# Kernel tuning notes

Hardware: AMD Instinct MI355X
Metric: run time of the kernel (lower is better)

The kernel has to match this reference:

```python
import jax, jax.numpy as jnp
import numpy as np

N = 100000   # nodes
E = 1600000  # edges
H = 2        # heads
F = 64       # out_feats per head
D = 256      # node feature dim
DE = 8       # edge feature dim
NEG_SLOPE = 0.2


def setup_inputs() -> dict:
    key = jax.random.key(0)
    ks = jax.random.split(key, 12)
    s = 0.05
    return {
        "feat_src": jax.random.normal(ks[0], (N, D), jnp.float32),
        "feat_edge": jax.random.normal(ks[1], (E, DE), jnp.float32),
        "edge_src": jax.random.randint(ks[2], (E,), 0, N, jnp.int32),
        "edge_dst": jax.random.randint(ks[3], (E,), 0, N, jnp.int32),
        "W_src": jax.random.normal(ks[4], (H * F, D), jnp.float32) * s,
        "W_dst": jax.random.normal(ks[5], (H * F, D), jnp.float32) * s,
        "b_dst": jax.random.normal(ks[6], (H * F,), jnp.float32) * s,
        "W_attn_src": jax.random.normal(ks[7], (H, D), jnp.float32) * s,
        "W_attn_dst": jax.random.normal(ks[8], (H, D), jnp.float32) * s,
        "W_attn_edge": jax.random.normal(ks[9], (H, DE), jnp.float32) * s,
        "W_ngnn": jax.random.normal(ks[10], (H * F, H * F), jnp.float32) * s,
        "b_ngnn": jax.random.normal(ks[11], (H * F,), jnp.float32) * s,
    }


def reference(feat_src, feat_edge, edge_src, edge_dst,
              W_src, W_dst, b_dst, W_attn_src, W_attn_dst, W_attn_edge,
              W_ngnn, b_ngnn):
    # node projections (graph is not a block -> feat_dst = feat_src)
    h_src = (feat_src @ W_src.T).reshape(N, H, F)          # [N,H,F]
    h_dst = (feat_src @ W_dst.T + b_dst).reshape(N, H, F)  # residual branch

    # per-node attention logits [N,H]
    a_src = feat_src @ W_attn_src.T
    a_dst = feat_src @ W_attn_dst.T
    a_edge = feat_edge @ W_attn_edge.T                     # [E,H]

    # per-edge score: u_add_v + edge term, LeakyReLU
    e = a_src[edge_src] + a_dst[edge_dst] + a_edge         # [E,H]
    e = jnp.where(e >= 0, e, NEG_SLOPE * e)

    # edge softmax over incoming edges of each destination node
    m = jax.ops.segment_max(e, edge_dst, num_segments=N)   # [N,H]
    ex = jnp.exp(e - m[edge_dst])
    z = jax.ops.segment_sum(ex, edge_dst, num_segments=N)  # [N,H]
    a = ex / z[edge_dst]                                   # [E,H]

    # weighted gather-scatter aggregation: u_mul_e -> sum per dst
    msg = h_src[edge_src] * a[:, :, None]                  # [E,H,F]
    rst = jax.ops.segment_sum(msg, edge_dst, num_segments=N)  # [N,H,F]

    # ngnn layer + ReLU
    rst = rst.reshape(N, H * F)
    rst = jax.nn.relu(rst @ W_ngnn.T + b_ngnn)
    rst = rst.reshape(N, H, F)

    # residual connection via dst_fc
    rst = rst + h_dst
    return rst
```

## Files before the change

kernel.cpp:

```cpp
#include <hip/hip_runtime.h>
#include <hip/hip_bf16.h>
#include <math.h>

#define NN 100000
#define EE 1600000
#define DD 256
#define DEE 8
#define HF 128
#define NEG_SLOPE 0.2f
#define NBUCK 196
#define P1_EPB 2048
#define P1_TPB 512
#define P1_ITER (P1_EPB / P1_TPB)

typedef __bf16 bf16x8 __attribute__((ext_vector_type(8)));
typedef float  f32x4  __attribute__((ext_vector_type(4)));

__device__ inline ushort f2bf(float f) {
    uint32_t x = __builtin_bit_cast(uint32_t, f);
    x += 0x7fffu + ((x >> 16) & 1u);
    return (ushort)(x >> 16);
}
__device__ inline float bf2f(ushort u) {
    uint32_t x = ((uint32_t)u) << 16;
    return __builtin_bit_cast(float, x);
}
__device__ inline float u2f(uint u) { return __builtin_bit_cast(float, u); }
__device__ inline uint f2u(float f) { return __builtin_bit_cast(uint, f); }
__device__ inline float lo_bf(uint p) { return __builtin_bit_cast(float, p << 16); }
__device__ inline float hi_bf(uint p) { return __builtin_bit_cast(float, p & 0xffff0000u); }

__device__ inline void load_lds16(const void* g, void* l) {
    __builtin_amdgcn_global_load_lds(
        (const __attribute__((address_space(1))) void*)g,
        (__attribute__((address_space(3))) void*)l, 16, 0, 0);
}

__global__ __launch_bounds__(256) void f2bf3_kernel(
    const float* __restrict__ wa, const float* __restrict__ wb,
    const float* __restrict__ wc,
    ushort* __restrict__ oa, ushort* __restrict__ ob, ushort* __restrict__ oc)
{
    int i = (blockIdx.x * 256 + threadIdx.x) * 4;
    const int na = HF * DD, nb2 = 2 * HF * DD, nc3 = 2 * HF * DD + HF * HF;
    const float* src; ushort* dst; int o;
    if (i < na)       { src = wa; dst = oa; o = i; }
    else if (i < nb2) { src = wb; dst = ob; o = i - na; }
    else if (i < nc3) { src = wc; dst = oc; o = i - nb2; }
    else return;
    float4 v = *(const float4*)(src + o);
    ushort4 u;
    u.x = f2bf(v.x); u.y = f2bf(v.y); u.z = f2bf(v.z); u.w = f2bf(v.w);
    *(ushort4*)(dst + o) = u;
}

template<int K>
__global__ __launch_bounds__(256) void mfma_gemm_dual(
    const ushort* __restrict__ W0,
    const ushort* __restrict__ W1,
    const ushort* __restrict__ Xb,
    const float*  __restrict__ bias1,
    ushort* __restrict__ out0, ushort* __restrict__ out1)
{
    __shared__ ushort As[2][128 * 32];
    __shared__ ushort Bs[64 * 32];

    const int tid  = threadIdx.x;
    const int lane = tid & 63, wv = tid >> 6;
    const int wm = wv >> 1, wn = wv & 1;
    const int r = lane & 15, quad = lane >> 4;
    const int m0 = blockIdx.x * 64;

    f32x4 acc[2][4][2] = {};

    for (int k0 = 0; k0 < K; k0 += 32) {
#pragma unroll
        for (int t = 0; t < 2; ++t) {
            int is  = wv + t * 4;
            int row = is * 16 + (lane >> 2);
            int ko  = k0 + (lane & 3) * 8;
            load_lds16(W0 + (size_t)row * K + ko, &As[0][is * 512]);
            load_lds16(W1 + (size_t)row * K + ko, &As[1][is * 512]);
        }
        {
            int is  = wv;
            int row = is * 16 + (lane >> 2);
            int ko  = k0 + (lane & 3) * 8;
            int gm = m0 + row; gm = gm < NN ? gm : NN - 1;
            load_lds16(Xb + (size_t)gm * K + ko, &Bs[is * 512]);
        }
        __syncthreads();
        bf16x8 a[2][4], b[2];
#pragma unroll
        for (int i = 0; i < 4; ++i) {
            a[0][i] = __builtin_bit_cast(bf16x8,
                      *(const f32x4*)&As[0][(wm * 64 + i * 16 + r) * 32 + quad * 8]);
            a[1][i] = __builtin_bit_cast(bf16x8,
                      *(const f32x4*)&As[1][(wm * 64 + i * 16 + r) * 32 + quad * 8]);
        }
#pragma unroll
        for (int j = 0; j < 2; ++j)
            b[j] = __builtin_bit_cast(bf16x8,
                   *(const f32x4*)&Bs[(wn * 32 + j * 16 + r) * 32 + quad * 8]);
#pragma unroll
        for (int s = 0; s < 2; ++s)
#pragma unroll
            for (int i = 0; i < 4; ++i)
#pragma unroll
                for (int j = 0; j < 2; ++j)
                    acc[s][i][j] = __builtin_amdgcn_mfma_f32_16x16x32_bf16(
                        a[s][i], b[j], acc[s][i][j], 0, 0, 0);
        __syncthreads();
    }

#pragma unroll
    for (int s = 0; s < 2; ++s) {
        ushort* outp = s ? out1 : out0;
#pragma unroll
        for (int i = 0; i < 4; ++i) {
            int fbase = wm * 64 + i * 16 + quad * 4;
            float4 bv = make_float4(0.f, 0.f, 0.f, 0.f);
            if (s == 1) bv = *(const float4*)(bias1 + fbase);
#pragma unroll
            for (int j = 0; j < 2; ++j) {
                int node = m0 + wn * 32 + j * 16 + r;
                if (node >= NN) continue;
                f32x4 v = acc[s][i][j];
                v[0] += bv.x; v[1] += bv.y; v[2] += bv.z; v[3] += bv.w;
                ushort4 o;
                o.x = f2bf(v[0]); o.y = f2bf(v[1]); o.z = f2bf(v[2]); o.w = f2bf(v[3]);
                *(ushort4*)(outp + (size_t)node * HF + fbase) = o;
            }
        }
    }
}

template<int K>
__global__ __launch_bounds__(256) void mfma_gemm_ngnn(
    const ushort* __restrict__ Wb,
    const ushort* __restrict__ Xb,
    const float*  __restrict__ bias,
    const ushort* __restrict__ resid,
    float* __restrict__ outp)
{
    __shared__ ushort As[128 * 32];
    __shared__ ushort Bs[128 * 32];

    const int tid  = threadIdx.x;
    const int lane = tid & 63, wv = tid >> 6;
    const int wm = wv >> 1, wn = wv & 1;
    const int r = lane & 15, quad = lane >> 4;
    const int m0 = blockIdx.x * 128;

    f32x4 acc[4][4] = {};

    for (int k0 = 0; k0 < K; k0 += 32) {
#pragma unroll
        for (int t = 0; t < 2; ++t) {
            int is  = wv + t * 4;
            int row = is * 16 + (lane >> 2);
            int ko  = k0 + (lane & 3) * 8;
            load_lds16(Wb + (size_t)row * K + ko, &As[is * 512]);
            int gm = m0 + row; gm = gm < NN ? gm : NN - 1;
            load_lds16(Xb + (size_t)gm * K + ko, &Bs[is * 512]);
        }
        __syncthreads();
        bf16x8 a[4], b[4];
#pragma unroll
        for (int i = 0; i < 4; ++i) {
            a[i] = __builtin_bit_cast(bf16x8,
                   *(const f32x4*)&As[(wm * 64 + i * 16 + r) * 32 + quad * 8]);
            b[i] = __builtin_bit_cast(bf16x8,
                   *(const f32x4*)&Bs[(wn * 64 + i * 16 + r) * 32 + quad * 8]);
        }
#pragma unroll
        for (int i = 0; i < 4; ++i)
#pragma unroll
            for (int j = 0; j < 4; ++j)
                acc[i][j] = __builtin_amdgcn_mfma_f32_16x16x32_bf16(
                    a[i], b[j], acc[i][j], 0, 0, 0);
        __syncthreads();
    }

#pragma unroll
    for (int i = 0; i < 4; ++i) {
        int fbase = wm * 64 + i * 16 + quad * 4;
        float4 bv = *(const float4*)(bias + fbase);
#pragma unroll
        for (int j = 0; j < 4; ++j) {
            int node = m0 + wn * 64 + j * 16 + r;
            if (node >= NN) continue;
            f32x4 v = acc[i][j];
            ushort4 rs = *(const ushort4*)(resid + (size_t)node * HF + fbase);
            float4 o;
            o.x = fmaxf(v[0] + bv.x, 0.f) + bf2f(rs.x);
            o.y = fmaxf(v[1] + bv.y, 0.f) + bf2f(rs.y);
            o.z = fmaxf(v[2] + bv.z, 0.f) + bf2f(rs.z);
            o.w = fmaxf(v[3] + bv.w, 0.f) + bf2f(rs.w);
            *(float4*)(outp + (size_t)node * HF + fbase) = o;
        }
    }
}

__global__ __launch_bounds__(256) void attn_logits_kernel(
    const float* __restrict__ feat,
    const float* __restrict__ Was, const float* __restrict__ Wad,
    float* __restrict__ a_src, float* __restrict__ a_dst,
    ushort* __restrict__ feat_bf)
{
    int wave = threadIdx.x >> 6, lane = threadIdx.x & 63;
    int node = blockIdx.x * 4 + wave;
    if (node >= NN) return;
    float4 f = *(const float4*)(feat + (size_t)node * DD + lane * 4);
    ushort4 fb;
    fb.x = f2bf(f.x); fb.y = f2bf(f.y); fb.z = f2bf(f.z); fb.w = f2bf(f.w);
    *(ushort4*)(feat_bf + (size_t)node * DD + lane * 4) = fb;

    float4 w0 = *(const float4*)(Was + 0 * DD + lane * 4);
    float4 w1 = *(const float4*)(Was + 1 * DD + lane * 4);
    float4 w2 = *(const float4*)(Wad + 0 * DD + lane * 4);
    float4 w3 = *(const float4*)(Wad + 1 * DD + lane * 4);
    float p0 = f.x * w0.x + f.y * w0.y + f.z * w0.z + f.w * w0.w;
    float p1 = f.x * w1.x + f.y * w1.y + f.z * w1.z + f.w * w1.w;
    float p2 = f.x * w2.x + f.y * w2.y + f.z * w2.z + f.w * w2.w;
    float p3 = f.x * w3.x + f.y * w3.y + f.z * w3.z + f.w * w3.w;
#pragma unroll
    for (int o = 32; o > 0; o >>= 1) {
        p0 += __shfl_xor(p0, o);
        p1 += __shfl_xor(p1, o);
        p2 += __shfl_xor(p2, o);
        p3 += __shfl_xor(p3, o);
    }
    if (lane == 0) {
        a_src[node * 2 + 0] = p0; a_src[node * 2 + 1] = p1;
        a_dst[node * 2 + 0] = p2; a_dst[node * 2 + 1] = p3;
    }
}

__global__ __launch_bounds__(256) void hist_kernel(
    const int* __restrict__ edge_dst, int* __restrict__ deg)
{
    int i = blockIdx.x * 256 + threadIdx.x;
    if (i < EE) atomicAdd(&deg[edge_dst[i]], 1);
}

#define SCAN_ELEMS 1024
__global__ __launch_bounds__(256) void scan1_kernel(
    const int* __restrict__ deg, int* __restrict__ offsets, int* __restrict__ blockSums)
{
    __shared__ int sd[256];
    int tid = threadIdx.x;
    int base = blockIdx.x * SCAN_ELEMS + tid * 4;
    int v[4];
#pragma unroll
    for (int c = 0; c < 4; ++c) v[c] = (base + c < NN) ? deg[base + c] : 0;
    int tsum = v[0] + v[1] + v[2] + v[3];
    sd[tid] = tsum;
    __syncthreads();
    for (int o = 1; o < 256; o <<= 1) {
        int x = (tid >= o) ? sd[tid - o] : 0;
        __syncthreads();
        sd[tid] += x;
        __syncthreads();
    }
    int excl = sd[tid] - tsum;
    int run = excl;
#pragma unroll
    for (int c = 0; c < 4; ++c) {
        if (base + c < NN) offsets[base + c] = run;
        run += v[c];
    }
    if (tid == 255) blockSums[blockIdx.x] = sd[255];
}

__global__ __launch_bounds__(128) void scan2_kernel(int* __restrict__ blockSums, int nb)
{
    __shared__ int sd[128];
    int tid = threadIdx.x;
    int tv = (tid < nb) ? blockSums[tid] : 0;
    sd[tid] = tv;
    __syncthreads();
    for (int o = 1; o < 128; o <<= 1) {
        int x = (tid >= o) ? sd[tid - o] : 0;
        __syncthreads();
        sd[tid] += x;
        __syncthreads();
    }
    if (tid < nb) blockSums[tid] = sd[tid] - tv;
}

__global__ __launch_bounds__(256) void scan3_kernel(
    int* __restrict__ offsets, const int* __restrict__ blockSums,
    int* __restrict__ bcur)
{
    int tid = threadIdx.x;
    int base = blockIdx.x * SCAN_ELEMS + tid * 4;
    int add = blockSums[blockIdx.x];
#pragma unroll
    for (int c = 0; c < 4; ++c) {
        int idx = base + c;
        if (idx < NN) {
            int v = offsets[idx] + add;
            offsets[idx] = v;
            if ((idx & 511) == 0) bcur[idx >> 9] = v;
        }
    }
    if (blockIdx.x == 0 && tid == 0) offsets[NN] = EE;
}

__global__ __launch_bounds__(P1_TPB) void bucket_scatter_kernel(
    const int* __restrict__ edge_src, const int* __restrict__ edge_dst,
    const float* __restrict__ feat_edge,
    const float* __restrict__ a_src, const float* __restrict__ a_dst,
    const float* __restrict__ Wae,
    int* __restrict__ bcur, uint4* __restrict__ staging)
{
    __shared__ uint4 rec[P1_EPB];
    __shared__ int cnt[256];
    __shared__ int scanv[256];
    __shared__ int cur[256];
    __shared__ int basearr[256];
    __shared__ int wsum[4];

    const int tid = threadIdx.x;
    const int lane = tid & 63;
    const int b0 = blockIdx.x * P1_EPB;

    if (tid < 256) cnt[tid] = 0;
    __syncthreads();

    int sA[P1_ITER], dA[P1_ITER];
#pragma unroll
    for (int j = 0; j < P1_ITER; ++j) {
        int i = b0 + j * P1_TPB + tid;
        int s = 0, d = 0;
        if (i < EE) {
            s = edge_src[i];
            d = edge_dst[i];
            atomicAdd(&cnt[d >> 9], 1);
        }
        sA[j] = s; dA[j] = d;
    }
    __syncthreads();

    int c = (tid < 256) ? cnt[tid] : 0;
    int x = c;
#pragma unroll
    for (int o = 1; o < 64; o <<= 1) {
        int y = __shfl_up(x, o);
        if (lane >= o) x += y;
    }
    if (tid < 256 && lane == 63) wsum[tid >> 6] = x;
    __syncthreads();
    if (tid < 256) {
        int w4 = tid >> 6;
        int add = 0;
        if (w4 > 0) add += wsum[0];
        if (w4 > 1) add += wsum[1];
        if (w4 > 2) add += wsum[2];
        int excl = x - c + add;
        cur[tid]   = excl;
        scanv[tid] = excl;
        if (tid < NBUCK) basearr[tid] = c ? atomicAdd(&bcur[tid], c) : 0;
    }
    __syncthreads();

    float4 w00 = ((const float4*)Wae)[0], w01 = ((const float4*)Wae)[1];
    float4 w10 = ((const float4*)Wae)[2], w11 = ((const float4*)Wae)[3];

    float4 e0v[P1_ITER], e1v[P1_ITER];
    float2 asv[P1_ITER], adv[P1_ITER];
#pragma unroll
    for (int j = 0; j < P1_ITER; ++j) {
        int i = b0 + j * P1_TPB + tid;
        if (i >= EE) continue;
        e0v[j] = ((const float4*)feat_edge)[i * 2 + 0];
        e1v[j] = ((const float4*)feat_edge)[i * 2 + 1];
        asv[j] = ((const float2*)a_src)[sA[j]];
        adv[j] = ((const float2*)a_dst)[dA[j]];
    }

#pragma unroll
    for (int j = 0; j < P1_ITER; ++j) {
        int i = b0 + j * P1_TPB + tid;
        if (i >= EE) continue;
        int s = sA[j], d = dA[j];
        float4 e0 = e0v[j], e1 = e1v[j];
        float ae0 = e0.x*w00.x + e0.y*w00.y + e0.z*w00.z + e0.w*w00.w
                  + e1.x*w01.x + e1.y*w01.y + e1.z*w01.z + e1.w*w01.w;
        float ae1 = e0.x*w10.x + e0.y*w10.y + e0.z*w10.z + e0.w*w10.w
                  + e1.x*w11.x + e1.y*w11.y + e1.z*w11.z + e1.w*w11.w;
        float v0 = asv[j].x + adv[j].x + ae0;
        float v1 = asv[j].y + adv[j].y + ae1;
        v0 = (v0 >= 0.f) ? v0 : NEG_SLOPE * v0;
        v1 = (v1 >= 0.f) ? v1 : NEG_SLOPE * v1;
        int bk = d >> 9;
        int pos = atomicAdd(&cur[bk], 1);
        rec[pos] = make_uint4((uint)s, (uint)d, f2u(v0), f2u(v1));
    }
    __syncthreads();

    const int tot = (EE - b0 < P1_EPB) ? (EE - b0) : P1_EPB;
    for (int idx = tid; idx < tot; idx += P1_TPB) {
        uint4 r = rec[idx];
        int bk = (int)(r.y >> 9);
        staging[basearr[bk] + (idx - scanv[bk])] = r;
    }
}

__global__ __launch_bounds__(1024) void fine_scatter_kernel(
    const int* __restrict__ offsets,
    const uint4* __restrict__ staging, uint4* __restrict__ pairs)
{
    __shared__ int cur[512];
    const int tid = threadIdx.x;
    const int nb0 = blockIdx.x * 512;
    const int ncnt = (NN - nb0 < 512) ? (NN - nb0) : 512;
    for (int i = tid; i < ncnt; i += 1024) cur[i] = offsets[nb0 + i];
    __syncthreads();
    const int lo = offsets[nb0];
    const int hi = offsets[nb0 + ncnt];
    for (int j = lo + tid; j < hi; j += 1024) {
        uint4 it = staging[j];
        int n = (int)it.y - nb0;
        int pos = atomicAdd(&cur[n], 1);
        pairs[pos] = it;
    }
}

__global__ __launch_bounds__(256) void aggregate_fused(
    const int* __restrict__ offsets,
    const uint4* __restrict__ pairs,
    const ushort* __restrict__ hsrc,
    ushort* __restrict__ agg)
{
    __shared__ uint4 stash[4][64];
    const int wave = threadIdx.x >> 6, lane = threadIdx.x & 63;
    const int node = blockIdx.x * 4 + wave;
    if (node >= NN) return;
    const int off = offsets[node], end = offsets[node + 1];
    const int n = end - off;
    const int q4 = lane & 15;
    const int grp = lane >> 4;
    const int h0 = (q4 < 8);
    uint4* agg4 = (uint4*)agg;
    if (n <= 0) {
        if (grp == 0) agg4[(size_t)node * 16 + q4] = make_uint4(0u, 0u, 0u, 0u);
        return;
    }
    const uint4* hp4 = (const uint4*)hsrc;

    float a0 = 0.f, a1 = 0.f, a2 = 0.f, a3 = 0.f;
    float a4 = 0.f, a5 = 0.f, a6 = 0.f, a7 = 0.f;
    float z0 = 0.f, z1 = 0.f;

    if (n <= 64) {
        uint4 pr = (lane < n) ? pairs[off + lane]
                              : make_uint4(0u, 0u, 0xff800000u, 0xff800000u);
        float m0 = u2f(pr.z), m1 = u2f(pr.w);
#pragma unroll
        for (int o = 32; o > 0; o >>= 1) {
            m0 = fmaxf(m0, __shfl_xor(m0, o));
            m1 = fmaxf(m1, __shfl_xor(m1, o));
        }
        float ex0 = (lane < n) ? __expf(u2f(pr.z) - m0) : 0.f;
        float ex1 = (lane < n) ? __expf(u2f(pr.w) - m1) : 0.f;
        z0 = ex0; z1 = ex1;
        stash[wave][lane] = make_uint4(pr.x, f2u(ex0), f2u(ex1), 0u);
        __builtin_amdgcn_wave_barrier();
        const int nt = (n + 3) >> 2;
#pragma unroll 4
        for (int t = 0; t < nt; ++t) {
            uint4 st = stash[wave][t * 4 + grp];
            float w = h0 ? u2f(st.y) : u2f(st.z);
            uint4 p = hp4[(size_t)st.x * 16 + q4];
            a0 = fmaf(w, lo_bf(p.x), a0); a1 = fmaf(w, hi_bf(p.x), a1);
            a2 = fmaf(w, lo_bf(p.y), a2); a3 = fmaf(w, hi_bf(p.y), a3);
            a4 = fmaf(w, lo_bf(p.z), a4); a5 = fmaf(w, hi_bf(p.z), a5);
            a6 = fmaf(w, lo_bf(p.w), a6); a7 = fmaf(w, hi_bf(p.w), a7);
        }
    } else {
        float m0 = -INFINITY, m1 = -INFINITY;
        for (int c0 = 0; c0 < n; c0 += 64) {
            if (c0 + lane < n) {
                uint4 pr = pairs[off + c0 + lane];
                m0 = fmaxf(m0, u2f(pr.z));
                m1 = fmaxf(m1, u2f(pr.w));
            }
        }
#pragma unroll
        for (int o = 32; o > 0; o >>= 1) {
            m0 = fmaxf(m0, __shfl_xor(m0, o));
            m1 = fmaxf(m1, __shfl_xor(m1, o));
        }
        for (int c0 = 0; c0 < n; c0 += 64) {
            int cn = n - c0; if (cn > 64) cn = 64;
            uint srcv = 0; float ex0 = 0.f, ex1 = 0.f;
            if (lane < cn) {
                uint4 pr = pairs[off + c0 + lane];
                srcv = pr.x;
                ex0 = __expf(u2f(pr.z) - m0);
                ex1 = __expf(u2f(pr.w) - m1);
                z0 += ex0; z1 += ex1;
            }
            __builtin_amdgcn_wave_barrier();
            stash[wave][lane] = make_uint4(srcv, f2u(ex0), f2u(ex1), 0u);
            __builtin_amdgcn_wave_barrier();
            const int nt = (cn + 3) >> 2;
#pragma unroll 4
            for (int t = 0; t < nt; ++t) {
                uint4 st = stash[wave][t * 4 + grp];
                float w = h0 ? u2f(st.y) : u2f(st.z);
                uint4 p = hp4[(size_t)st.x * 16 + q4];
                a0 = fmaf(w, lo_bf(p.x), a0); a1 = fmaf(w, hi_bf(p.x), a1);
                a2 = fmaf(w, lo_bf(p.y), a2); a3 = fmaf(w, hi_bf(p.y), a3);
                a4 = fmaf(w, lo_bf(p.z), a4); a5 = fmaf(w, hi_bf(p.z), a5);
                a6 = fmaf(w, lo_bf(p.w), a6); a7 = fmaf(w, hi_bf(p.w), a7);
            }
            __builtin_amdgcn_wave_barrier();
        }
    }

#pragma unroll
    for (int o = 32; o >= 16; o >>= 1) {
        a0 += __shfl_xor(a0, o); a1 += __shfl_xor(a1, o);
        a2 += __shfl_xor(a2, o); a3 += __shfl_xor(a3, o);
        a4 += __shfl_xor(a4, o); a5 += __shfl_xor(a5, o);
        a6 += __shfl_xor(a6, o); a7 += __shfl_xor(a7, o);
    }
#pragma unroll
    for (int o = 32; o > 0; o >>= 1) {
        z0 += __shfl_xor(z0, o);
        z1 += __shfl_xor(z1, o);
    }
    float zi = h0 ? ((z0 > 0.f) ? 1.f / z0 : 0.f)
                  : ((z1 > 0.f) ? 1.f / z1 : 0.f);
    if (grp == 0) {
        uint4 o4;
        o4.x = ((uint)f2bf(a1 * zi) << 16) | (uint)f2bf(a0 * zi);
        o4.y = ((uint)f2bf(a3 * zi) << 16) | (uint)f2bf(a2 * zi);
        o4.z = ((uint)f2bf(a5 * zi) << 16) | (uint)f2bf(a4 * zi);
        o4.w = ((uint)f2bf(a7 * zi) << 16) | (uint)f2bf(a6 * zi);
        agg4[(size_t)node * 16 + q4] = o4;
    }
}

extern "C" void kernel_launch(void* const* d_in, const int* in_sizes, int n_in,
                              void* d_out, int out_size, void* d_ws, size_t ws_size,
                              hipStream_t stream) {
    (void)in_sizes; (void)n_in; (void)out_size; (void)ws_size;
    const float* feat_src  = (const float*)d_in[0];
    const float* feat_edge = (const float*)d_in[1];
    const int*   edge_src  = (const int*)d_in[2];
    const int*   edge_dst  = (const int*)d_in[3];
    const float* W_src     = (const float*)d_in[4];
    const float* W_dst     = (const float*)d_in[5];
    const float* b_dst     = (const float*)d_in[6];
    const float* W_attn_src  = (const float*)d_in[7];
    const float* W_attn_dst  = (const float*)d_in[8];
    const float* W_attn_edge = (const float*)d_in[9];
    const float* W_ngnn    = (const float*)d_in[10];
    const float* b_ngnn    = (const float*)d_in[11];
    float* out = (float*)d_out;

    char* base = (char*)d_ws;
    size_t off = 0;
    auto take = [&](size_t bytes) -> void* {
        void* p = base + off;
        off = (off + bytes + 511) & ~(size_t)511;
        return p;
    };
    ushort* feat_bf  = (ushort*)take((size_t)NN * DD * 2);
    ushort* h_src_bf = (ushort*)take((size_t)NN * HF * 2);
    uint4*  staging  = (uint4*)take((size_t)EE * 16);
    uint4*  pairs    = (uint4*)take((size_t)EE * 16);
    float*  a_src_b  = (float*)take((size_t)NN * 2 * 4);
    float*  a_dst_b  = (float*)take((size_t)NN * 2 * 4);
    int*    deg      = (int*)take((size_t)NN * 4);
    int*    offsets  = (int*)take((size_t)(NN + 1) * 4);
    int*    bcur     = (int*)take((size_t)NBUCK * 4);
    int*    blockSums= (int*)take(512);
    ushort* Wsrc_bf  = (ushort*)take((size_t)HF * DD * 2);
    ushort* Wdst_bf  = (ushort*)take((size_t)HF * DD * 2);
    ushort* Wngnn_bf = (ushort*)take((size_t)HF * HF * 2);
    ushort* h_dst_bf = (ushort*)staging;
    ushort* agg_bf   = feat_bf;

    const int NB_SCAN = (NN + SCAN_ELEMS - 1) / SCAN_ELEMS;
    const int GB_E  = (EE + 255) / 256;
    const int GB_M  = (NN + 127) / 128;
    const int GB_M64= (NN + 63) / 64;
    const int GB_N4 = (NN + 3) / 4;
    const int GB_P1 = (EE + P1_EPB - 1) / P1_EPB;
    const int W3_N  = (2 * HF * DD + HF * HF) / 4;
    const int GB_W3 = (W3_N + 255) / 256;

    hipMemsetAsync(deg, 0, (size_t)NN * 4, stream);
    hipLaunchKernelGGL(hist_kernel, dim3(GB_E), dim3(256), 0, stream, edge_dst, deg);
    hipLaunchKernelGGL(scan1_kernel, dim3(NB_SCAN), dim3(256), 0, stream, deg, offsets, blockSums);
    hipLaunchKernelGGL(scan2_kernel, dim3(1), dim3(128), 0, stream, blockSums, NB_SCAN);
    hipLaunchKernelGGL(scan3_kernel, dim3(NB_SCAN), dim3(256), 0, stream, offsets, blockSums, bcur);

    hipLaunchKernelGGL(attn_logits_kernel, dim3(GB_N4), dim3(256), 0, stream,
                       feat_src, W_attn_src, W_attn_dst, a_src_b, a_dst_b, feat_bf);

    hipLaunchKernelGGL(f2bf3_kernel, dim3(GB_W3), dim3(256), 0, stream,
                       W_src, W_dst, W_ngnn, Wsrc_bf, Wdst_bf, Wngnn_bf);

    hipLaunchKernelGGL(bucket_scatter_kernel, dim3(GB_P1), dim3(P1_TPB), 0, stream,
                       edge_src, edge_dst, feat_edge, a_src_b, a_dst_b, W_attn_edge,
                       bcur, staging);
    hipLaunchKernelGGL(fine_scatter_kernel, dim3(NBUCK), dim3(1024), 0, stream,
                       offsets, staging, pairs);

    hipLaunchKernelGGL((mfma_gemm_dual<DD>), dim3(GB_M64), dim3(256), 0, stream,
                       Wsrc_bf, Wdst_bf, feat_bf, b_dst, h_src_bf, h_dst_bf);

    hipLaunchKernelGGL(aggregate_fused, dim3(GB_N4), dim3(256), 0, stream,
                       offsets, pairs, h_src_bf, agg_bf);

    hipLaunchKernelGGL(mfma_gemm_ngnn<HF>, dim3(GB_M), dim3(256), 0, stream,
                       Wngnn_bf, agg_bf, b_ngnn, h_dst_bf, out);
}
```

Baseline: 491.6 us.

## Fuse attention logits and bf16 feature conversion into dual projection GEMM

Removes the separate attention-logit kernel that wrote a bf16 copy of the node features. The dual GEMM now loads fp32 features directly, converts them into a full-K LDS tile (8 slices), and computes the four attention dot products from the same loads. The GEMM moves ahead of the edge scatter so the logits exist before bucket_scatter. This saves the round trip of the bf16 feature buffer and one launch. The cost is much more LDS per block (about 36KB), which may lower occupancy, and h_dst and agg now need their own workspace buffers.

```diff
diff --git a/kernel.cpp b/kernel.cpp
--- a/kernel.cpp
+++ b/kernel.cpp
@@ -55,15 +55,19 @@
 }
 
 template<int K>
-__global__ __launch_bounds__(256) void mfma_gemm_dual(
+__global__ __launch_bounds__(256) void gemm_dual_attn(
     const ushort* __restrict__ W0,
     const ushort* __restrict__ W1,
-    const ushort* __restrict__ Xb,
+    const float*  __restrict__ Xf,
+    const float*  __restrict__ Was,
+    const float*  __restrict__ Wad,
     const float*  __restrict__ bias1,
+    float* __restrict__ a_src, float* __restrict__ a_dst,
     ushort* __restrict__ out0, ushort* __restrict__ out1)
 {
     __shared__ ushort As[2][128 * 32];
-    __shared__ ushort Bs[64 * 32];
+    __shared__ ushort Bsf[8][64 * 32];
+    __shared__ float  wlds[4][K];
 
     const int tid  = threadIdx.x;
     const int lane = tid & 63, wv = tid >> 6;
@@ -71,8 +75,57 @@
     const int r = lane & 15, quad = lane >> 4;
     const int m0 = blockIdx.x * 64;
 
+    {
+        int vec = tid >> 6, e = (tid & 63) * 4;
+        const float* src = (vec < 2) ? (Was + vec * K + e) : (Wad + (vec - 2) * K + e);
+        *(float4*)&wlds[vec][e] = *(const float4*)src;
+    }
+    __syncthreads();
+
+    const int node = tid >> 2;
+    const int kq   = (tid & 3) * 8;
+    int gm = m0 + node; gm = gm < NN ? gm : NN - 1;
+    const float* frow = Xf + (size_t)gm * K;
+    float p0 = 0.f, p1 = 0.f, p2 = 0.f, p3 = 0.f;
+#pragma unroll
+    for (int st = 0; st < 8; ++st) {
+        int k = st * 32 + kq;
+        float4 fa = *(const float4*)(frow + k);
+        float4 fb = *(const float4*)(frow + k + 4);
+        uint q0 = ((uint)f2bf(fa.y) << 16) | f2bf(fa.x);
+        uint q1 = ((uint)f2bf(fa.w) << 16) | f2bf(fa.z);
+        uint q2 = ((uint)f2bf(fb.y) << 16) | f2bf(fb.x);
+        uint q3 = ((uint)f2bf(fb.w) << 16) | f2bf(fb.z);
+        *(uint4*)&Bsf[st][node * 32 + kq] = make_uint4(q0, q1, q2, q3);
+
+        float4 wv0a = *(const float4*)&wlds[0][k];
+        float4 wv0b = *(const float4*)&wlds[0][k + 4];
+        float4 wv1a = *(const float4*)&wlds[1][k];
+        float4 wv1b = *(const float4*)&wlds[1][k + 4];
+        float4 wv2a = *(const float4*)&wlds[2][k];
+        float4 wv2b = *(const float4*)&wlds[2][k + 4];
+        float4 wv3a = *(const float4*)&wlds[3][k];
+        float4 wv3b = *(const float4*)&wlds[3][k + 4];
+        p0 += fa.x*wv0a.x + fa.y*wv0a.y + fa.z*wv0a.z + fa.w*wv0a.w
+            + fb.x*wv0b.x + fb.y*wv0b.y + fb.z*wv0b.z + fb.w*wv0b.w;
+        p1 += fa.x*wv1a.x + fa.y*wv1a.y + fa.z*wv1a.z + fa.w*wv1a.w
+            + fb.x*wv1b.x + fb.y*wv1b.y + fb.z*wv1b.z + fb.w*wv1b.w;
+        p2 += fa.x*wv2a.x + fa.y*wv2a.y + fa.z*wv2a.z + fa.w*wv2a.w
+            + fb.x*wv2b.x + fb.y*wv2b.y + fb.z*wv2b.z + fb.w*wv2b.w;
+        p3 += fa.x*wv3a.x + fa.y*wv3a.y + fa.z*wv3a.z + fa.w*wv3a.w
+            + fb.x*wv3b.x + fb.y*wv3b.y + fb.z*wv3b.z + fb.w*wv3b.w;
+    }
+    p0 += __shfl_xor(p0, 1); p0 += __shfl_xor(p0, 2);
+    p1 += __shfl_xor(p1, 1); p1 += __shfl_xor(p1, 2);
+    p2 += __shfl_xor(p2, 1); p2 += __shfl_xor(p2, 2);
+    p3 += __shfl_xor(p3, 1); p3 += __shfl_xor(p3, 2);
+    if ((tid & 3) == 0 && m0 + node < NN) {
+        *(float2*)&a_src[(size_t)(m0 + node) * 2] = make_float2(p0, p1);
+        *(float2*)&a_dst[(size_t)(m0 + node) * 2] = make_float2(p2, p3);
+    }
+    __syncthreads();
+
     f32x4 acc[2][4][2] = {};
-
     for (int k0 = 0; k0 < K; k0 += 32) {
 #pragma unroll
         for (int t = 0; t < 2; ++t) {
@@ -82,13 +135,6 @@
             load_lds16(W0 + (size_t)row * K + ko, &As[0][is * 512]);
             load_lds16(W1 + (size_t)row * K + ko, &As[1][is * 512]);
         }
-        {
-            int is  = wv;
-            int row = is * 16 + (lane >> 2);
-            int ko  = k0 + (lane & 3) * 8;
-            int gm = m0 + row; gm = gm < NN ? gm : NN - 1;
-            load_lds16(Xb + (size_t)gm * K + ko, &Bs[is * 512]);
-        }
         __syncthreads();
         bf16x8 a[2][4], b[2];
 #pragma unroll
@@ -101,7 +147,7 @@
 #pragma unroll
         for (int j = 0; j < 2; ++j)
             b[j] = __builtin_bit_cast(bf16x8,
-                   *(const f32x4*)&Bs[(wn * 32 + j * 16 + r) * 32 + quad * 8]);
+                   *(const f32x4*)&Bsf[k0 >> 5][(wn * 32 + j * 16 + r) * 32 + quad * 8]);
 #pragma unroll
         for (int s = 0; s < 2; ++s)
 #pragma unroll
@@ -123,13 +169,13 @@
             if (s == 1) bv = *(const float4*)(bias1 + fbase);
 #pragma unroll
             for (int j = 0; j < 2; ++j) {
-                int node = m0 + wn * 32 + j * 16 + r;
-                if (node >= NN) continue;
+                int node2 = m0 + wn * 32 + j * 16 + r;
+                if (node2 >= NN) continue;
                 f32x4 v = acc[s][i][j];
                 v[0] += bv.x; v[1] += bv.y; v[2] += bv.z; v[3] += bv.w;
                 ushort4 o;
                 o.x = f2bf(v[0]); o.y = f2bf(v[1]); o.z = f2bf(v[2]); o.w = f2bf(v[3]);
-                *(ushort4*)(outp + (size_t)node * HF + fbase) = o;
+                *(ushort4*)(outp + (size_t)node2 * HF + fbase) = o;
             }
         }
     }
@@ -199,41 +245,6 @@
             o.w = fmaxf(v[3] + bv.w, 0.f) + bf2f(rs.w);
             *(float4*)(outp + (size_t)node * HF + fbase) = o;
         }
-    }
-}
-
-__global__ __launch_bounds__(256) void attn_logits_kernel(
-    const float* __restrict__ feat,
-    const float* __restrict__ Was, const float* __restrict__ Wad,
-    float* __restrict__ a_src, float* __restrict__ a_dst,
-    ushort* __restrict__ feat_bf)
-{
-    int wave = threadIdx.x >> 6, lane = threadIdx.x & 63;
-    int node = blockIdx.x * 4 + wave;
-    if (node >= NN) return;
-    float4 f = *(const float4*)(feat + (size_t)node * DD + lane * 4);
-    ushort4 fb;
-    fb.x = f2bf(f.x); fb.y = f2bf(f.y); fb.z = f2bf(f.z); fb.w = f2bf(f.w);
-    *(ushort4*)(feat_bf + (size_t)node * DD + lane * 4) = fb;
-
-    float4 w0 = *(const float4*)(Was + 0 * DD + lane * 4);
-    float4 w1 = *(const float4*)(Was + 1 * DD + lane * 4);
-    float4 w2 = *(const float4*)(Wad + 0 * DD + lane * 4);
-    float4 w3 = *(const float4*)(Wad + 1 * DD + lane * 4);
-    float p0 = f.x * w0.x + f.y * w0.y + f.z * w0.z + f.w * w0.w;
-    float p1 = f.x * w1.x + f.y * w1.y + f.z * w1.z + f.w * w1.w;
-    float p2 = f.x * w2.x + f.y * w2.y + f.z * w2.z + f.w * w2.w;
-    float p3 = f.x * w3.x + f.y * w3.y + f.z * w3.z + f.w * w3.w;
-#pragma unroll
-    for (int o = 32; o > 0; o >>= 1) {
-        p0 += __shfl_xor(p0, o);
-        p1 += __shfl_xor(p1, o);
-        p2 += __shfl_xor(p2, o);
-        p3 += __shfl_xor(p3, o);
-    }
-    if (lane == 0) {
-        a_src[node * 2 + 0] = p0; a_src[node * 2 + 1] = p1;
-        a_dst[node * 2 + 0] = p2; a_dst[node * 2 + 1] = p3;
     }
 }
 
@@ -570,8 +581,9 @@
         off = (off + bytes + 511) & ~(size_t)511;
         return p;
     };
-    ushort* feat_bf  = (ushort*)take((size_t)NN * DD * 2);
     ushort* h_src_bf = (ushort*)take((size_t)NN * HF * 2);
+    ushort* h_dst_bf = (ushort*)take((size_t)NN * HF * 2);
+    ushort* agg_bf   = (ushort*)take((size_t)NN * HF * 2);
     uint4*  staging  = (uint4*)take((size_t)EE * 16);
     uint4*  pairs    = (uint4*)take((size_t)EE * 16);
     float*  a_src_b  = (float*)take((size_t)NN * 2 * 4);
@@ -583,8 +595,6 @@
     ushort* Wsrc_bf  = (ushort*)take((size_t)HF * DD * 2);
     ushort* Wdst_bf  = (ushort*)take((size_t)HF * DD * 2);
     ushort* Wngnn_bf = (ushort*)take((size_t)HF * HF * 2);
-    ushort* h_dst_bf = (ushort*)staging;
-    ushort* agg_bf   = feat_bf;
 
     const int NB_SCAN = (NN + SCAN_ELEMS - 1) / SCAN_ELEMS;
     const int GB_E  = (EE + 255) / 256;
@@ -601,11 +611,12 @@
     hipLaunchKernelGGL(scan2_kernel, dim3(1), dim3(128), 0, stream, blockSums, NB_SCAN);
     hipLaunchKernelGGL(scan3_kernel, dim3(NB_SCAN), dim3(256), 0, stream, offsets, blockSums, bcur);
 
-    hipLaunchKernelGGL(attn_logits_kernel, dim3(GB_N4), dim3(256), 0, stream,
-                       feat_src, W_attn_src, W_attn_dst, a_src_b, a_dst_b, feat_bf);
-
     hipLaunchKernelGGL(f2bf3_kernel, dim3(GB_W3), dim3(256), 0, stream,
                        W_src, W_dst, W_ngnn, Wsrc_bf, Wdst_bf, Wngnn_bf);
+
+    hipLaunchKernelGGL((gemm_dual_attn<DD>), dim3(GB_M64), dim3(256), 0, stream,
+                       Wsrc_bf, Wdst_bf, feat_src, W_attn_src, W_attn_dst, b_dst,
+                       a_src_b, a_dst_b, h_src_bf, h_dst_bf);
 
     hipLaunchKernelGGL(bucket_scatter_kernel, dim3(GB_P1), dim3(P1_TPB), 0, stream,
                        edge_src, edge_dst, feat_edge, a_src_b, a_dst_b, W_attn_edge,
@@ -613,9 +624,6 @@
     hipLaunchKernelGGL(fine_scatter_kernel, dim3(NBUCK), dim3(1024), 0, stream,
                        offsets, staging, pairs);
 
-    hipLaunchKernelGGL((mfma_gemm_dual<DD>), dim3(GB_M64), dim3(256), 0, stream,
-                       Wsrc_bf, Wdst_bf, feat_bf, b_dst, h_src_bf, h_dst_bf);
-
     hipLaunchKernelGGL(aggregate_fused, dim3(GB_N4), dim3(256), 0, stream,
                        offsets, pairs, h_src_bf, agg_bf);
 
```

After: 518.8 us. 1.06x slower.
